# Kernel optimization log

Hardware: AMD Instinct MI355X
Metric: run time of the kernel (lower is better)

Reference implementation:

```python
import jax, jax.numpy as jnp
import numpy as np

N_GENE, N_DRUG = 20000, 3000
D_GENE, D_DRUG = 1024, 512
H = [256, 128]
E_GG, E_DD, E_DT = 600000, 120000, 150000
P_DROP = 0.2


def _dropout(x, key):
    # F.dropout(p=0.2, training=True) with a fixed key for determinism
    keep = jax.random.bernoulli(key, 1.0 - P_DROP, x.shape)
    return jnp.where(keep, x / (1.0 - P_DROP), 0.0).astype(x.dtype)


def _gcn_norm(x, W, b, edge_index, n):
    src, dst = edge_index[0], edge_index[1]
    loops = jnp.arange(n, dtype=src.dtype)
    src = jnp.concatenate([src, loops])
    dst = jnp.concatenate([dst, loops])
    deg = jax.ops.segment_sum(jnp.ones(src.shape, x.dtype), dst, num_segments=n)
    dinv = jax.lax.rsqrt(deg)  # deg >= 1 thanks to self loops
    xw = x @ W  # [n_src, out]
    msg = xw[src] * (dinv[src] * dinv[dst])[:, None]  # [E+n, out]
    return jax.ops.segment_sum(msg, dst, num_segments=n) + b


def _gcn_plain(x, W, b, edge_index, n_dst):
    # PyG GCNConv(add_self_loops=False, normalize=False): A X W + b (bipartite scatter)
    xw = x @ W
    return jax.ops.segment_sum(xw[edge_index[0]], edge_index[1], num_segments=n_dst) + b


def _l2norm(x):
    # F.normalize(dim=1, p=2), eps=1e-12
    n = jnp.linalg.norm(x, axis=1, keepdims=True)
    return x / jnp.maximum(n, 1e-12)


def setup_inputs() -> dict:
    key = jax.random.key(0)
    ks = jax.random.split(key, 32)
    inp = {}
    inp["gene_feat"] = jax.random.normal(ks[0], (N_GENE, D_GENE), jnp.float32)
    inp["drug_feat"] = jax.random.normal(ks[1], (N_DRUG, D_DRUG), jnp.float32)
    inp["ei_gg"] = jax.random.randint(ks[2], (2, E_GG), 0, N_GENE)
    inp["ei_dd"] = jax.random.randint(ks[3], (2, E_DD), 0, N_DRUG)
    # drug_target: messages from drug (src row) to gene (dst row)
    inp["ei_dt"] = jnp.stack([jax.random.randint(ks[4], (E_DT,), 0, N_DRUG),
                               jax.random.randint(ks[5], (E_DT,), 0, N_GENE)])
    # target_drug: messages from gene (src row) to drug (dst row)
    inp["ei_td"] = jnp.stack([jax.random.randint(ks[6], (E_DT,), 0, N_GENE),
                               jax.random.randint(ks[7], (E_DT,), 0, N_DRUG)])
    dims_in = {"gg": D_GENE, "dd": D_DRUG, "dt": D_DRUG, "td": D_GENE}
    i = 8
    for l, h in enumerate(H):
        for et in ["gg", "dd", "dt", "td"]:
            din = dims_in[et] if l == 0 else H[l - 1]
            s = float(1.0 / np.sqrt(din))
            inp[f"W{l}_{et}"] = jax.random.uniform(ks[i], (din, h), jnp.float32, -s, s)
            i += 1
            inp[f"b{l}_{et}"] = jnp.zeros((h,), jnp.float32)
    return inp


def reference(gene_feat, drug_feat, ei_gg, ei_dd, ei_dt, ei_td,
              W0_gg, b0_gg, W0_dd, b0_dd, W0_dt, b0_dt, W0_td, b0_td,
              W1_gg, b1_gg, W1_dd, b1_dd, W1_dt, b1_dt, W1_td, b1_td):
    dk = jax.random.split(jax.random.key(42), 8)
    layers = [
        ((W0_gg, b0_gg), (W0_dd, b0_dd), (W0_dt, b0_dt), (W0_td, b0_td)),
        ((W1_gg, b1_gg), (W1_dd, b1_dd), (W1_dt, b1_dt), (W1_td, b1_td)),
    ]
    xg, xd = gene_feat, drug_feat
    k = 0
    for (Wgg, bgg), (Wdd, bdd), (Wdt, bdt), (Wtd, btd) in layers:
        gg = jax.nn.relu(_gcn_norm(_dropout(xg, dk[k + 0]), Wgg, bgg, ei_gg, N_GENE))
        dd = jax.nn.relu(_gcn_norm(_dropout(xd, dk[k + 1]), Wdd, bdd, ei_dd, N_DRUG))
        dt = jax.nn.relu(_gcn_plain(_dropout(xd, dk[k + 2]), Wdt, bdt, ei_dt, N_GENE))
        td = jax.nn.relu(_gcn_plain(_dropout(xg, dk[k + 3]), Wtd, btd, ei_td, N_DRUG))
        # per-edge-type L2 normalize, then sum contributions per node type
        xg = _l2norm(gg) + _l2norm(dt)
        xd = _l2norm(dd) + _l2norm(td)
        k += 4
    # concat node-type outputs: genes first, drugs second -> [N_GENE+N_DRUG, H[-1]]
    return jnp.concatenate([xg, xd], axis=0)
```

## Files before the change

### kernel.cpp

```cpp
#include <hip/hip_runtime.h>
#include <stdint.h>

#define N_GENE 20000
#define N_DRUG 3000
#define D_GENE 1024
#define D_DRUG 512
#define H0 256
#define H1 128
#define E_GG 600000
#define E_DD 120000
#define E_DT 150000

typedef __attribute__((ext_vector_type(8))) short bf16x8;
typedef __attribute__((ext_vector_type(4))) float f32x4;

__host__ __device__ inline uint32_t rotl32(uint32_t x, int d) {
#ifdef __HIP_DEVICE_COMPILE__
    return __builtin_amdgcn_alignbit(x, x, 32 - d);
#else
    return (x << d) | (x >> (32 - d));
#endif
}

__host__ __device__ inline void tf2x32(uint32_t k0, uint32_t k1, uint32_t x0, uint32_t x1,
                                       uint32_t& o0, uint32_t& o1) {
    uint32_t ks2 = k0 ^ k1 ^ 0x1BD11BDAu;
    x0 += k0; x1 += k1;
#define TFR(r) { x0 += x1; x1 = rotl32(x1, r); x1 ^= x0; }
    TFR(13) TFR(15) TFR(26) TFR(6)
    x0 += k1; x1 += ks2 + 1u;
    TFR(17) TFR(29) TFR(16) TFR(24)
    x0 += ks2; x1 += k0 + 2u;
    TFR(13) TFR(15) TFR(26) TFR(6)
    x0 += k0; x1 += k1 + 3u;
    TFR(17) TFR(29) TFR(16) TFR(24)
    x0 += k1; x1 += ks2 + 4u;
    TFR(13) TFR(15) TFR(26) TFR(6)
    x0 += ks2; x1 += k0 + 5u;
#undef TFR
    o0 = x0; o1 = x1;
}

__device__ inline short f2bf(float f) {
    uint32_t u = __float_as_uint(f);
    uint32_t r = (u + 0x7FFFu + ((u >> 16) & 1u)) >> 16;
    return (short)r;
}
__device__ inline float bf_lo(uint32_t u) { return __uint_as_float(u << 16); }
__device__ inline float bf_hi(uint32_t u) { return __uint_as_float(u & 0xFFFF0000u); }

#define CUM_E0 600000u
#define CUM_E1 720000u
#define CUM_E2 870000u
#define CUM_E3 1020000u

struct Cast4P {
    unsigned c0, c1, c2, c3;
    uint32_t k0a, k1a, k0b, k1b, k0c, k1c, k0d, k1d;
};
__global__ __launch_bounds__(256) void cast4_kernel(
    const float* __restrict__ Xg, const float* __restrict__ Xd,
    short* __restrict__ Am, Cast4P P, int castBlocks,
    const int* __restrict__ gg, const int* __restrict__ dd,
    const int* __restrict__ dt, const int* __restrict__ td, int* __restrict__ cnt) {
    int bx = blockIdx.x;
    if (bx >= castBlocks) {
        unsigned e = (unsigned)(bx - castBlocks) * 256u + threadIdx.x;
        if (e >= CUM_E3) return;
        const int* dsts; unsigned base, noff;
        if (e >= CUM_E2)      { dsts = td + E_DT; base = CUM_E2; noff = 43000; }
        else if (e >= CUM_E1) { dsts = dt + E_DT; base = CUM_E1; noff = 23000; }
        else if (e >= CUM_E0) { dsts = dd + E_DD; base = CUM_E0; noff = 20000; }
        else                  { dsts = gg + E_GG; base = 0;      noff = 0; }
        atomicAdd(&cnt[noff + dsts[e - base]], 1);
        return;
    }
    unsigned j = ((unsigned)bx * 256u + threadIdx.x) * 8u;
    if (j >= P.c3) return;
    unsigned base; uint32_t k0, k1; const float* X;
    if (j >= P.c2)      { base = P.c2; k0 = P.k0d; k1 = P.k1d; X = Xd; }
    else if (j >= P.c1) { base = P.c1; k0 = P.k0c; k1 = P.k1c; X = Xd; }
    else if (j >= P.c0) { base = P.c0; k0 = P.k0b; k1 = P.k1b; X = Xg; }
    else                { base = 0u;   k0 = P.k0a; k1 = P.k1a; X = Xg; }
    unsigned local = j - base;
    float4 xa = *(const float4*)(X + local);
    float4 xb = *(const float4*)(X + local + 4);
    float xv[8] = {xa.x, xa.y, xa.z, xa.w, xb.x, xb.y, xb.z, xb.w};
    union { short s[8]; uint4 u; } st;
#pragma unroll
    for (int i = 0; i < 8; i++) {
        uint32_t a, b;
        tf2x32(k0, k1, 0u, local + (unsigned)i, a, b);
        uint32_t bits = a ^ b;
        st.s[i] = ((bits >> 9) < 6710887u) ? f2bf(xv[i] * 1.25f) : (short)0;
    }
    *(uint4*)(Am + j) = st.u;
}

__global__ __launch_bounds__(1024) void scan_p1(const int* __restrict__ cnt,
                                                int* __restrict__ tmp, int* __restrict__ bsum) {
    __shared__ int buf[1024];
    int tid = threadIdx.x;
    int i = blockIdx.x * 1024 + tid;
    int v = (i < 46000) ? cnt[i] : 0;
    buf[tid] = v;
    __syncthreads();
    for (int off = 1; off < 1024; off <<= 1) {
        int t = (tid >= off) ? buf[tid - off] : 0;
        __syncthreads();
        buf[tid] += t;
        __syncthreads();
    }
    if (i < 46000) tmp[i] = buf[tid];
    if (tid == 1023) bsum[blockIdx.x] = buf[1023];
}

__global__ void scan_p2(int* __restrict__ bsum) {
    int lane = threadIdx.x;
    int v = (lane < 45) ? bsum[lane] : 0;
    int orig = v;
    for (int off = 1; off < 64; off <<= 1) {
        int t = __shfl_up(v, off, 64);
        if (lane >= off) v += t;
    }
    if (lane < 45) bsum[lane] = v - orig;
}

__global__ __launch_bounds__(1024) void scan_p3(const int* __restrict__ cnt,
                                                const int* __restrict__ tmp,
                                                const int* __restrict__ bsum,
                                                int* __restrict__ rpall, int* __restrict__ pos,
                                                float* __restrict__ dinv_g,
                                                float* __restrict__ dinv_d) {
    int i = blockIdx.x * 1024 + threadIdx.x;
    if (i < 46000) {
        int g = tmp[i] - cnt[i] + bsum[blockIdx.x];
        rpall[i] = g;
        pos[i] = g;
        if (i < 20000) dinv_g[i] = 1.0f / sqrtf((float)cnt[i] + 1.0f);
        else if (i < 23000) dinv_d[i - 20000] = 1.0f / sqrtf((float)cnt[i] + 1.0f);
    }
    if (i == 0) rpall[46000] = (int)CUM_E3;
}

struct CastT4P {
    unsigned c0, c1, c2, c3;
    int lgK0, lgK1, lgK2, lgK3;
    int N;
};
__global__ __launch_bounds__(256) void fillcastT_kernel(
    const int* __restrict__ gg, const int* __restrict__ dd,
    const int* __restrict__ dt, const int* __restrict__ td,
    int* __restrict__ pos, int* __restrict__ col,
    const float* __restrict__ W0, const float* __restrict__ W1,
    const float* __restrict__ W2, const float* __restrict__ W3,
    short* __restrict__ Wt, CastT4P P, int fillBlocks) {
    int bx = blockIdx.x;
    if (bx < fillBlocks) {
        unsigned e = (unsigned)bx * 256u + threadIdx.x;
        if (e >= CUM_E3) return;
        const int* ei; unsigned base, noff; int E;
        if (e >= CUM_E2)      { ei = td; base = CUM_E2; noff = 43000; E = E_DT; }
        else if (e >= CUM_E1) { ei = dt; base = CUM_E1; noff = 23000; E = E_DT; }
        else if (e >= CUM_E0) { ei = dd; base = CUM_E0; noff = 20000; E = E_DD; }
        else                  { ei = gg; base = 0;      noff = 0;     E = E_GG; }
        unsigned local = e - base;
        int src = ei[local], dst = ei[E + local];
        int p = atomicAdd(&pos[noff + dst], 1);
        col[p] = src;
        return;
    }
    unsigned idx = (unsigned)(bx - fillBlocks) * 256u + threadIdx.x;
    if (idx >= P.c3) return;
    unsigned base; const float* W; int lgK;
    if (idx >= P.c2)      { base = P.c2; W = W3; lgK = P.lgK3; }
    else if (idx >= P.c1) { base = P.c1; W = W2; lgK = P.lgK2; }
    else if (idx >= P.c0) { base = P.c0; W = W1; lgK = P.lgK1; }
    else                  { base = 0u;   W = W0; lgK = P.lgK0; }
    unsigned local = idx - base;
    unsigned n = local >> lgK, k = local & ((1u << lgK) - 1u);
    Wt[idx] = f2bf(W[(size_t)k * P.N + n]);
}

__global__ __launch_bounds__(256) void castT4_kernel(
    const float* __restrict__ W0, const float* __restrict__ W1,
    const float* __restrict__ W2, const float* __restrict__ W3,
    short* __restrict__ Wt, CastT4P P) {
    unsigned idx = blockIdx.x * 256u + threadIdx.x;
    if (idx >= P.c3) return;
    unsigned base; const float* W; int lgK;
    if (idx >= P.c2)      { base = P.c2; W = W3; lgK = P.lgK3; }
    else if (idx >= P.c1) { base = P.c1; W = W2; lgK = P.lgK2; }
    else if (idx >= P.c0) { base = P.c0; W = W1; lgK = P.lgK1; }
    else                  { base = 0u;   W = W0; lgK = P.lgK0; }
    unsigned local = idx - base;
    unsigned n = local >> lgK, k = local & ((1u << lgK) - 1u);
    Wt[idx] = f2bf(W[(size_t)k * P.N + n]);
}

struct GDesc { unsigned aoff, boff, coff; const float* rs; int M, K, mb0; };
#define LDP 72
__global__ __launch_bounds__(256) void gemm4_kernel(
    const short* __restrict__ Ab, const short* __restrict__ Wb, short* __restrict__ Cb,
    GDesc d0, GDesc d1, GDesc d2, GDesc d3, int N) {
    __shared__ short As[64 * LDP];
    __shared__ short Bs[64 * LDP];
    GDesc d;
    int bx = blockIdx.x;
    if (bx >= d3.mb0) d = d3;
    else if (bx >= d2.mb0) d = d2;
    else if (bx >= d1.mb0) d = d1;
    else d = d0;
    bx -= d.mb0;
    const short* A = Ab + d.aoff;
    const short* Bt = Wb + d.boff;
    short* C = Cb + d.coff;
    const int M = d.M, K = d.K;

    int tid = threadIdx.x;
    int lane = tid & 63;
    int w = tid >> 6;
    int m = lane & 15, kb = lane >> 4;
    int m0w = (w >> 1) * 32, n0w = (w & 1) * 32;
    int gm = bx * 64, gn = blockIdx.y * 64;

    int flat0 = tid, flat1 = tid + 256;
    int ar0 = flat0 >> 3, ac0 = (flat0 & 7) * 8;
    int ar1 = flat1 >> 3, ac1 = (flat1 & 7) * 8;
    int agr0 = min(gm + ar0, M - 1), agr1 = min(gm + ar1, M - 1);
    const short* pa0 = A + (size_t)agr0 * K + ac0;
    const short* pa1 = A + (size_t)agr1 * K + ac1;
    const short* pb0 = Bt + (size_t)(gn + ar0) * K + ac0;
    const short* pb1 = Bt + (size_t)(gn + ar1) * K + ac1;

    f32x4 acc[2][2];
#pragma unroll
    for (int i = 0; i < 2; i++)
#pragma unroll
        for (int j = 0; j < 2; j++) acc[i][j] = (f32x4){0.f, 0.f, 0.f, 0.f};

    uint4 ra0 = *(const uint4*)pa0;
    uint4 ra1 = *(const uint4*)pa1;
    uint4 rb0 = *(const uint4*)pb0;
    uint4 rb1 = *(const uint4*)pb1;

    int nt = K >> 6;
    for (int t = 0; t < nt; ++t) {
        __syncthreads();
        *(uint4*)&As[ar0 * LDP + ac0] = ra0;
        *(uint4*)&As[ar1 * LDP + ac1] = ra1;
        *(uint4*)&Bs[ar0 * LDP + ac0] = rb0;
        *(uint4*)&Bs[ar1 * LDP + ac1] = rb1;
        __syncthreads();
        if (t + 1 < nt) {
            int kt = (t + 1) << 6;
            ra0 = *(const uint4*)(pa0 + kt);
            ra1 = *(const uint4*)(pa1 + kt);
            rb0 = *(const uint4*)(pb0 + kt);
            rb1 = *(const uint4*)(pb1 + kt);
        }
#pragma unroll
        for (int ks = 0; ks < 2; ++ks) {
            bf16x8 a0 = *(const bf16x8*)&As[(m0w + m) * LDP + ks * 32 + kb * 8];
            bf16x8 a1 = *(const bf16x8*)&As[(m0w + 16 + m) * LDP + ks * 32 + kb * 8];
            bf16x8 b0 = *(const bf16x8*)&Bs[(n0w + m) * LDP + ks * 32 + kb * 8];
            bf16x8 b1 = *(const bf16x8*)&Bs[(n0w + 16 + m) * LDP + ks * 32 + kb * 8];
            acc[0][0] = __builtin_amdgcn_mfma_f32_16x16x32_bf16(a0, b0, acc[0][0], 0, 0, 0);
            acc[0][1] = __builtin_amdgcn_mfma_f32_16x16x32_bf16(a0, b1, acc[0][1], 0, 0, 0);
            acc[1][0] = __builtin_amdgcn_mfma_f32_16x16x32_bf16(a1, b0, acc[1][0], 0, 0, 0);
            acc[1][1] = __builtin_amdgcn_mfma_f32_16x16x32_bf16(a1, b1, acc[1][1], 0, 0, 0);
        }
    }
#pragma unroll
    for (int mf = 0; mf < 2; ++mf)
#pragma unroll
        for (int j = 0; j < 4; ++j) {
            int r = gm + m0w + mf * 16 + kb * 4 + j;
            if (r < M) {
                float s = d.rs ? d.rs[r] : 1.0f;
#pragma unroll
                for (int nf = 0; nf < 2; ++nf)
                    C[(size_t)r * N + gn + n0w + nf * 16 + m] = f2bf(acc[mf][nf][j] * s);
            }
        }
}

template <int F>
__global__ __launch_bounds__(256) void agg2_kernel(
    const short* __restrict__ XWa, const int* __restrict__ rpa,
    const float* __restrict__ dinv, const float* __restrict__ ba,
    const short* __restrict__ XWb2, const int* __restrict__ rpb,
    const float* __restrict__ bb, const int* __restrict__ col,
    float* __restrict__ out, int n_dst) {
    const int h = 64 * F;
    int lane = threadIdx.x & 63;
    int row = blockIdx.x * 4 + (threadIdx.x >> 6);
    if (row >= n_dst) return;
    int c0 = lane * F;
    float acc[F], va[F];

#pragma unroll
    for (int i = 0; i < F; i++) acc[i] = 0.f;
    {
        if constexpr (F == 4) {
            uint2 u = *(const uint2*)(XWa + (size_t)row * h + c0);
            acc[0] += bf_lo(u.x); acc[1] += bf_hi(u.x);
            acc[2] += bf_lo(u.y); acc[3] += bf_hi(u.y);
        } else {
            uint32_t u = *(const uint32_t*)(XWa + (size_t)row * h + c0);
            acc[0] += bf_lo(u); acc[1] += bf_hi(u);
        }
        int s0 = rpa[row], s1 = rpa[row + 1];
        int p = s0;
        for (; p + 8 <= s1; p += 8) {
            int c[8];
#pragma unroll
            for (int i = 0; i < 8; i++) c[i] = col[p + i];
            if constexpr (F == 4) {
                uint2 g[8];
#pragma unroll
                for (int i = 0; i < 8; i++) g[i] = *(const uint2*)(XWa + (size_t)c[i] * h + c0);
#pragma unroll
                for (int i = 0; i < 8; i++) {
                    acc[0] += bf_lo(g[i].x); acc[1] += bf_hi(g[i].x);
                    acc[2] += bf_lo(g[i].y); acc[3] += bf_hi(g[i].y);
                }
            } else {
                uint32_t g[8];
#pragma unroll
                for (int i = 0; i < 8; i++) g[i] = *(const uint32_t*)(XWa + (size_t)c[i] * h + c0);
#pragma unroll
                for (int i = 0; i < 8; i++) { acc[0] += bf_lo(g[i]); acc[1] += bf_hi(g[i]); }
            }
        }
        for (; p < s1; p++) {
            int s = col[p];
            if constexpr (F == 4) {
                uint2 u = *(const uint2*)(XWa + (size_t)s * h + c0);
                acc[0] += bf_lo(u.x); acc[1] += bf_hi(u.x);
                acc[2] += bf_lo(u.y); acc[3] += bf_hi(u.y);
            } else {
                uint32_t u = *(const uint32_t*)(XWa + (size_t)s * h + c0);
                acc[0] += bf_lo(u); acc[1] += bf_hi(u);
            }
        }
    }
    float mul = dinv[row];
    float ssa = 0.f;
#pragma unroll
    for (int i = 0; i < F; i++) {
        float v = fmaxf(acc[i] * mul + ba[c0 + i], 0.f);
        va[i] = v;
        ssa += v * v;
    }

#pragma unroll
    for (int i = 0; i < F; i++) acc[i] = 0.f;
    {
        int s0 = rpb[row], s1 = rpb[row + 1];
        int p = s0;
        for (; p + 8 <= s1; p += 8) {
            int c[8];
#pragma unroll
            for (int i = 0; i < 8; i++) c[i] = col[p + i];
            if constexpr (F == 4) {
                uint2 g[8];
#pragma unroll
                for (int i = 0; i < 8; i++) g[i] = *(const uint2*)(XWb2 + (size_t)c[i] * h + c0);
#pragma unroll
                for (int i = 0; i < 8; i++) {
                    acc[0] += bf_lo(g[i].x); acc[1] += bf_hi(g[i].x);
                    acc[2] += bf_lo(g[i].y); acc[3] += bf_hi(g[i].y);
                }
            } else {
                uint32_t g[8];
#pragma unroll
                for (int i = 0; i < 8; i++) g[i] = *(const uint32_t*)(XWb2 + (size_t)c[i] * h + c0);
#pragma unroll
                for (int i = 0; i < 8; i++) { acc[0] += bf_lo(g[i]); acc[1] += bf_hi(g[i]); }
            }
        }
        for (; p < s1; p++) {
            int s = col[p];
            if constexpr (F == 4) {
                uint2 u = *(const uint2*)(XWb2 + (size_t)s * h + c0);
                acc[0] += bf_lo(u.x); acc[1] += bf_hi(u.x);
                acc[2] += bf_lo(u.y); acc[3] += bf_hi(u.y);
            } else {
                uint32_t u = *(const uint32_t*)(XWb2 + (size_t)s * h + c0);
                acc[0] += bf_lo(u); acc[1] += bf_hi(u);
            }
        }
    }
    float ssb = 0.f;
#pragma unroll
    for (int i = 0; i < F; i++) {
        float v = fmaxf(acc[i] + bb[c0 + i], 0.f);
        acc[i] = v;
        ssb += v * v;
    }

#pragma unroll
    for (int off = 32; off >= 1; off >>= 1) {
        ssa += __shfl_xor(ssa, off, 64);
        ssb += __shfl_xor(ssb, off, 64);
    }
    float sa = 1.0f / fmaxf(sqrtf(ssa), 1e-12f);
    float sb = 1.0f / fmaxf(sqrtf(ssb), 1e-12f);
    float* orow = out + (size_t)row * h + c0;
    if constexpr (F == 4) {
        *(float4*)orow = make_float4(va[0] * sa + acc[0] * sb, va[1] * sa + acc[1] * sb,
                                     va[2] * sa + acc[2] * sb, va[3] * sa + acc[3] * sb);
    } else {
        *(float2*)orow = make_float2(va[0] * sa + acc[0] * sb, va[1] * sa + acc[1] * sb);
    }
}

extern "C" void kernel_launch(void* const* d_in, const int* in_sizes, int n_in,
                              void* d_out, int out_size, void* d_ws, size_t ws_size,
                              hipStream_t stream) {
    const float* gene = (const float*)d_in[0];
    const float* drug = (const float*)d_in[1];
    const int* ei_gg = (const int*)d_in[2];
    const int* ei_dd = (const int*)d_in[3];
    const int* ei_dt = (const int*)d_in[4];
    const int* ei_td = (const int*)d_in[5];
    const float* W0gg = (const float*)d_in[6];  const float* b0gg = (const float*)d_in[7];
    const float* W0dd = (const float*)d_in[8];  const float* b0dd = (const float*)d_in[9];
    const float* W0dt = (const float*)d_in[10]; const float* b0dt = (const float*)d_in[11];
    const float* W0td = (const float*)d_in[12]; const float* b0td = (const float*)d_in[13];
    const float* W1gg = (const float*)d_in[14]; const float* b1gg = (const float*)d_in[15];
    const float* W1dd = (const float*)d_in[16]; const float* b1dd = (const float*)d_in[17];
    const float* W1dt = (const float*)d_in[18]; const float* b1dt = (const float*)d_in[19];
    const float* W1td = (const float*)d_in[20]; const float* b1td = (const float*)d_in[21];

    uint32_t dk[8][2];
    for (uint32_t i = 0; i < 8; i++) tf2x32(0u, 42u, 0u, i, dk[i][0], dk[i][1]);

    char* p = (char*)d_ws;
    auto take = [&](size_t bytes) -> void* {
        void* r = (void*)p;
        p += (bytes + 255) & ~(size_t)255;
        return r;
    };
    short* Am   = (short*)take(sizeof(short) * 44032000ULL);
    short* XW   = (short*)take(sizeof(short) * 11776000ULL);
    short* Wt   = (short*)take(sizeof(short) * 786432ULL);
    float* xg1  = (float*)take(sizeof(float) * (size_t)N_GENE * H0);
    float* xd1  = (float*)take(sizeof(float) * (size_t)N_DRUG * H0);
    float* dinv_g = (float*)take(sizeof(float) * N_GENE);
    float* dinv_d = (float*)take(sizeof(float) * N_DRUG);
    int* cnt   = (int*)take(4 * 46000);
    int* tmp   = (int*)take(4 * 46000);
    int* bsum  = (int*)take(4 * 64);
    int* pos   = (int*)take(4 * 46000);
    int* rpall = (int*)take(4 * 46001);
    int* col   = (int*)take(4 * 1020000);

    const int* rp_gg = rpall;
    const int* rp_dd = rpall + 20000;
    const int* rp_dt = rpall + 23000;
    const int* rp_td = rpall + 43000;

    hipMemsetAsync(cnt, 0, 4 * 46000, stream);

    {
        Cast4P cp = {20480000u, 40960000u, 42496000u, 44032000u,
                     dk[0][0], dk[0][1], dk[3][0], dk[3][1],
                     dk[1][0], dk[1][1], dk[2][0], dk[2][1]};
        int castBlocks = 44032000 / 8 / 256;
        int countBlocks = (1020000 + 255) / 256;
        cast4_kernel<<<castBlocks + countBlocks, 256, 0, stream>>>(
            gene, drug, Am, cp, castBlocks, ei_gg, ei_dd, ei_dt, ei_td, cnt);
        scan_p1<<<45, 1024, 0, stream>>>(cnt, tmp, bsum);
        scan_p2<<<1, 64, 0, stream>>>(bsum);
        scan_p3<<<45, 1024, 0, stream>>>(cnt, tmp, bsum, rpall, pos, dinv_g, dinv_d);
        CastT4P tp = {262144u, 524288u, 655360u, 786432u, 10, 10, 9, 9, H0};
        int fillBlocks = (1020000 + 255) / 256;
        fillcastT_kernel<<<fillBlocks + (786432 + 255) / 256, 256, 0, stream>>>(
            ei_gg, ei_dd, ei_dt, ei_td, pos, col,
            W0gg, W0td, W0dd, W0dt, Wt, tp, fillBlocks);
        GDesc g0 = {0u,        0u,      0u,        dinv_g,  N_GENE, 1024, 0};
        GDesc g1 = {20480000u, 262144u, 5120000u,  nullptr, N_GENE, 1024, 313};
        GDesc g2 = {40960000u, 524288u, 10240000u, dinv_d,  N_DRUG, 512,  626};
        GDesc g3 = {42496000u, 655360u, 11008000u, nullptr, N_DRUG, 512,  673};
        gemm4_kernel<<<dim3(720, H0 / 64), 256, 0, stream>>>(Am, Wt, XW, g0, g1, g2, g3, H0);
        agg2_kernel<4><<<(N_GENE + 3) / 4, 256, 0, stream>>>(
            XW, rp_gg, dinv_g, b0gg, XW + 11008000, rp_dt, b0dt, col, xg1, N_GENE);
        agg2_kernel<4><<<(N_DRUG + 3) / 4, 256, 0, stream>>>(
            XW + 10240000, rp_dd, dinv_d, b0dd, XW + 5120000, rp_td, b0td, col, xd1, N_DRUG);
    }

    {
        Cast4P cp = {5120000u, 10240000u, 11008000u, 11776000u,
                     dk[4][0], dk[4][1], dk[7][0], dk[7][1],
                     dk[5][0], dk[5][1], dk[6][0], dk[6][1]};
        int castBlocks = 11776000 / 8 / 256;
        cast4_kernel<<<castBlocks, 256, 0, stream>>>(
            xg1, xd1, Am, cp, castBlocks, nullptr, nullptr, nullptr, nullptr, nullptr);
        CastT4P tp = {32768u, 65536u, 98304u, 131072u, 8, 8, 8, 8, H1};
        castT4_kernel<<<(131072 + 255) / 256, 256, 0, stream>>>(W1gg, W1td, W1dd, W1dt, Wt, tp);
        GDesc g0 = {0u,        0u,     0u,        dinv_g,  N_GENE, 256, 0};
        GDesc g1 = {5120000u,  32768u, 5120000u,  nullptr, N_GENE, 256, 313};
        GDesc g2 = {10240000u, 65536u, 10240000u, dinv_d,  N_DRUG, 256, 626};
        GDesc g3 = {11008000u, 98304u, 11008000u, nullptr, N_DRUG, 256, 673};
        gemm4_kernel<<<dim3(720, H1 / 64), 256, 0, stream>>>(Am, Wt, XW, g0, g1, g2, g3, H1);
        float* og = (float*)d_out;
        float* od = og + (size_t)N_GENE * H1;
        agg2_kernel<2><<<(N_GENE + 3) / 4, 256, 0, stream>>>(
            XW, rp_gg, dinv_g, b1gg, XW + 11008000, rp_dt, b1dt, col, og, N_GENE);
        agg2_kernel<2><<<(N_DRUG + 3) / 4, 256, 0, stream>>>(
            XW + 10240000, rp_dd, dinv_d, b1dd, XW + 5120000, rp_td, b1td, col, od, N_DRUG);
    }
}
```

Baseline: 421.3 us.

## Fuse dropout mask and bf16 cast into GEMM A-tile loads with full-N tiles

Removes the separate cast kernel that wrote a large dropout-masked bf16 copy of the activations. The GEMM now reads the fp32 features directly and computes the Threefry dropout mask inside the A-tile load. Each block covers the full output width (256 or 128) with 512 threads, so every A row is loaded once instead of once per 64-column tile. The cost is that the Threefry hashing now sits inside the GEMM's load path, fp32 A loads are twice as wide, and register use per thread goes up.

```diff
diff --git a/kernel.cpp b/kernel.cpp
--- a/kernel.cpp
+++ b/kernel.cpp
@@ -49,42 +49,7 @@
 __device__ inline float bf_lo(uint32_t u) { return __uint_as_float(u << 16); }
 __device__ inline float bf_hi(uint32_t u) { return __uint_as_float(u & 0xFFFF0000u); }
 
-#define CUM_E0 600000u
-#define CUM_E1 720000u
-#define CUM_E2 870000u
-#define CUM_E3 1020000u
-
-struct Cast4P {
-    unsigned c0, c1, c2, c3;
-    uint32_t k0a, k1a, k0b, k1b, k0c, k1c, k0d, k1d;
-};
-__global__ __launch_bounds__(256) void cast4_kernel(
-    const float* __restrict__ Xg, const float* __restrict__ Xd,
-    short* __restrict__ Am, Cast4P P, int castBlocks,
-    const int* __restrict__ gg, const int* __restrict__ dd,
-    const int* __restrict__ dt, const int* __restrict__ td, int* __restrict__ cnt) {
-    int bx = blockIdx.x;
-    if (bx >= castBlocks) {
-        unsigned e = (unsigned)(bx - castBlocks) * 256u + threadIdx.x;
-        if (e >= CUM_E3) return;
-        const int* dsts; unsigned base, noff;
-        if (e >= CUM_E2)      { dsts = td + E_DT; base = CUM_E2; noff = 43000; }
-        else if (e >= CUM_E1) { dsts = dt + E_DT; base = CUM_E1; noff = 23000; }
-        else if (e >= CUM_E0) { dsts = dd + E_DD; base = CUM_E0; noff = 20000; }
-        else                  { dsts = gg + E_GG; base = 0;      noff = 0; }
-        atomicAdd(&cnt[noff + dsts[e - base]], 1);
-        return;
-    }
-    unsigned j = ((unsigned)bx * 256u + threadIdx.x) * 8u;
-    if (j >= P.c3) return;
-    unsigned base; uint32_t k0, k1; const float* X;
-    if (j >= P.c2)      { base = P.c2; k0 = P.k0d; k1 = P.k1d; X = Xd; }
-    else if (j >= P.c1) { base = P.c1; k0 = P.k0c; k1 = P.k1c; X = Xd; }
-    else if (j >= P.c0) { base = P.c0; k0 = P.k0b; k1 = P.k1b; X = Xg; }
-    else                { base = 0u;   k0 = P.k0a; k1 = P.k1a; X = Xg; }
-    unsigned local = j - base;
-    float4 xa = *(const float4*)(X + local);
-    float4 xb = *(const float4*)(X + local + 4);
+__device__ inline uint4 maskpack8(float4 xa, float4 xb, unsigned local, uint32_t k0, uint32_t k1) {
     float xv[8] = {xa.x, xa.y, xa.z, xa.w, xb.x, xb.y, xb.z, xb.w};
     union { short s[8]; uint4 u; } st;
 #pragma unroll
@@ -94,7 +59,25 @@
         uint32_t bits = a ^ b;
         st.s[i] = ((bits >> 9) < 6710887u) ? f2bf(xv[i] * 1.25f) : (short)0;
     }
-    *(uint4*)(Am + j) = st.u;
+    return st.u;
+}
+
+#define CUM_E0 600000u
+#define CUM_E1 720000u
+#define CUM_E2 870000u
+#define CUM_E3 1020000u
+
+__global__ void count4_kernel(const int* __restrict__ gg, const int* __restrict__ dd,
+                              const int* __restrict__ dt, const int* __restrict__ td,
+                              int* __restrict__ cnt) {
+    unsigned e = blockIdx.x * 256u + threadIdx.x;
+    if (e >= CUM_E3) return;
+    const int* dsts; unsigned base, noff;
+    if (e >= CUM_E2)      { dsts = td + E_DT; base = CUM_E2; noff = 43000; }
+    else if (e >= CUM_E1) { dsts = dt + E_DT; base = CUM_E1; noff = 23000; }
+    else if (e >= CUM_E0) { dsts = dd + E_DD; base = CUM_E0; noff = 20000; }
+    else                  { dsts = gg + E_GG; base = 0;      noff = 0; }
+    atomicAdd(&cnt[noff + dsts[e - base]], 1);
 }
 
 __global__ __launch_bounds__(1024) void scan_p1(const int* __restrict__ cnt,
@@ -198,77 +181,86 @@
     Wt[idx] = f2bf(W[(size_t)k * P.N + n]);
 }
 
-struct GDesc { unsigned aoff, boff, coff; const float* rs; int M, K, mb0; };
+struct GDescF { const float* X; unsigned boff, coff; const float* rs; int M, K, mb0; uint32_t k0, k1; };
 #define LDP 72
-__global__ __launch_bounds__(256) void gemm4_kernel(
-    const short* __restrict__ Ab, const short* __restrict__ Wb, short* __restrict__ Cb,
-    GDesc d0, GDesc d1, GDesc d2, GDesc d3, int N) {
+template <int BN>
+__global__ __launch_bounds__(512) void gemm4f_kernel(
+    const short* __restrict__ Wb, short* __restrict__ Cb,
+    GDescF d0, GDescF d1, GDescF d2, GDescF d3) {
+    constexpr int WN = BN / 4;
+    constexpr int NF = WN / 16;
+    constexpr int SB = BN / 64;
     __shared__ short As[64 * LDP];
-    __shared__ short Bs[64 * LDP];
-    GDesc d;
+    __shared__ short Bs[BN * LDP];
+    GDescF d;
     int bx = blockIdx.x;
     if (bx >= d3.mb0) d = d3;
     else if (bx >= d2.mb0) d = d2;
     else if (bx >= d1.mb0) d = d1;
     else d = d0;
     bx -= d.mb0;
-    const short* A = Ab + d.aoff;
+    const int M = d.M, K = d.K;
     const short* Bt = Wb + d.boff;
     short* C = Cb + d.coff;
-    const int M = d.M, K = d.K;
 
     int tid = threadIdx.x;
-    int lane = tid & 63;
-    int w = tid >> 6;
+    int lane = tid & 63, w = tid >> 6;
     int m = lane & 15, kb = lane >> 4;
-    int m0w = (w >> 1) * 32, n0w = (w & 1) * 32;
-    int gm = bx * 64, gn = blockIdx.y * 64;
-
-    int flat0 = tid, flat1 = tid + 256;
-    int ar0 = flat0 >> 3, ac0 = (flat0 & 7) * 8;
-    int ar1 = flat1 >> 3, ac1 = (flat1 & 7) * 8;
-    int agr0 = min(gm + ar0, M - 1), agr1 = min(gm + ar1, M - 1);
-    const short* pa0 = A + (size_t)agr0 * K + ac0;
-    const short* pa1 = A + (size_t)agr1 * K + ac1;
-    const short* pb0 = Bt + (size_t)(gn + ar0) * K + ac0;
-    const short* pb1 = Bt + (size_t)(gn + ar1) * K + ac1;
-
-    f32x4 acc[2][2];
+    int m0w = (w >> 2) * 32, n0w = (w & 3) * WN;
+    int gm = bx * 64;
+
+    int ar = tid >> 3, ac = (tid & 7) * 8;
+    int agr = min(gm + ar, M - 1);
+    const float* pax = d.X + (size_t)agr * K + ac;
+    unsigned alocal = (unsigned)agr * (unsigned)K + (unsigned)ac;
+
+    int brr[SB], bcc[SB];
+    const short* pb[SB];
+#pragma unroll
+    for (int i = 0; i < SB; i++) {
+        int flat = tid + 512 * i;
+        brr[i] = flat >> 3; bcc[i] = (flat & 7) * 8;
+        pb[i] = Bt + (size_t)brr[i] * K + bcc[i];
+    }
+
+    f32x4 acc[2][NF];
 #pragma unroll
     for (int i = 0; i < 2; i++)
 #pragma unroll
-        for (int j = 0; j < 2; j++) acc[i][j] = (f32x4){0.f, 0.f, 0.f, 0.f};
-
-    uint4 ra0 = *(const uint4*)pa0;
-    uint4 ra1 = *(const uint4*)pa1;
-    uint4 rb0 = *(const uint4*)pb0;
-    uint4 rb1 = *(const uint4*)pb1;
+        for (int j = 0; j < NF; j++) acc[i][j] = (f32x4){0.f, 0.f, 0.f, 0.f};
+
+    float4 xa = *(const float4*)pax;
+    float4 xb = *(const float4*)(pax + 4);
+    uint4 rb[SB];
+#pragma unroll
+    for (int i = 0; i < SB; i++) rb[i] = *(const uint4*)pb[i];
+    uint4 a8 = maskpack8(xa, xb, alocal, d.k0, d.k1);
 
     int nt = K >> 6;
     for (int t = 0; t < nt; ++t) {
         __syncthreads();
-        *(uint4*)&As[ar0 * LDP + ac0] = ra0;
-        *(uint4*)&As[ar1 * LDP + ac1] = ra1;
-        *(uint4*)&Bs[ar0 * LDP + ac0] = rb0;
-        *(uint4*)&Bs[ar1 * LDP + ac1] = rb1;
+        *(uint4*)&As[ar * LDP + ac] = a8;
+#pragma unroll
+        for (int i = 0; i < SB; i++) *(uint4*)&Bs[brr[i] * LDP + bcc[i]] = rb[i];
         __syncthreads();
         if (t + 1 < nt) {
             int kt = (t + 1) << 6;
-            ra0 = *(const uint4*)(pa0 + kt);
-            ra1 = *(const uint4*)(pa1 + kt);
-            rb0 = *(const uint4*)(pb0 + kt);
-            rb1 = *(const uint4*)(pb1 + kt);
+            xa = *(const float4*)(pax + kt);
+            xb = *(const float4*)(pax + kt + 4);
+#pragma unroll
+            for (int i = 0; i < SB; i++) rb[i] = *(const uint4*)(pb[i] + kt);
+            a8 = maskpack8(xa, xb, alocal + (unsigned)kt, d.k0, d.k1);
         }
 #pragma unroll
         for (int ks = 0; ks < 2; ++ks) {
             bf16x8 a0 = *(const bf16x8*)&As[(m0w + m) * LDP + ks * 32 + kb * 8];
             bf16x8 a1 = *(const bf16x8*)&As[(m0w + 16 + m) * LDP + ks * 32 + kb * 8];
-            bf16x8 b0 = *(const bf16x8*)&Bs[(n0w + m) * LDP + ks * 32 + kb * 8];
-            bf16x8 b1 = *(const bf16x8*)&Bs[(n0w + 16 + m) * LDP + ks * 32 + kb * 8];
-            acc[0][0] = __builtin_amdgcn_mfma_f32_16x16x32_bf16(a0, b0, acc[0][0], 0, 0, 0);
-            acc[0][1] = __builtin_amdgcn_mfma_f32_16x16x32_bf16(a0, b1, acc[0][1], 0, 0, 0);
-            acc[1][0] = __builtin_amdgcn_mfma_f32_16x16x32_bf16(a1, b0, acc[1][0], 0, 0, 0);
-            acc[1][1] = __builtin_amdgcn_mfma_f32_16x16x32_bf16(a1, b1, acc[1][1], 0, 0, 0);
+#pragma unroll
+            for (int nf = 0; nf < NF; nf++) {
+                bf16x8 bf = *(const bf16x8*)&Bs[(n0w + nf * 16 + m) * LDP + ks * 32 + kb * 8];
+                acc[0][nf] = __builtin_amdgcn_mfma_f32_16x16x32_bf16(a0, bf, acc[0][nf], 0, 0, 0);
+                acc[1][nf] = __builtin_amdgcn_mfma_f32_16x16x32_bf16(a1, bf, acc[1][nf], 0, 0, 0);
+            }
         }
     }
 #pragma unroll
@@ -279,8 +271,8 @@
             if (r < M) {
                 float s = d.rs ? d.rs[r] : 1.0f;
 #pragma unroll
-                for (int nf = 0; nf < 2; ++nf)
-                    C[(size_t)r * N + gn + n0w + nf * 16 + m] = f2bf(acc[mf][nf][j] * s);
+                for (int nf = 0; nf < NF; ++nf)
+                    C[(size_t)r * BN + n0w + nf * 16 + m] = f2bf(acc[mf][nf][j] * s);
             }
         }
 }
@@ -443,7 +435,6 @@
         p += (bytes + 255) & ~(size_t)255;
         return r;
     };
-    short* Am   = (short*)take(sizeof(short) * 44032000ULL);
     short* XW   = (short*)take(sizeof(short) * 11776000ULL);
     short* Wt   = (short*)take(sizeof(short) * 786432ULL);
     float* xg1  = (float*)take(sizeof(float) * (size_t)N_GENE * H0);
@@ -463,28 +454,22 @@
     const int* rp_td = rpall + 43000;
 
     hipMemsetAsync(cnt, 0, 4 * 46000, stream);
+    count4_kernel<<<(1020000 + 255) / 256, 256, 0, stream>>>(ei_gg, ei_dd, ei_dt, ei_td, cnt);
+    scan_p1<<<45, 1024, 0, stream>>>(cnt, tmp, bsum);
+    scan_p2<<<1, 64, 0, stream>>>(bsum);
+    scan_p3<<<45, 1024, 0, stream>>>(cnt, tmp, bsum, rpall, pos, dinv_g, dinv_d);
+    CastT4P tp0 = {262144u, 524288u, 655360u, 786432u, 10, 10, 9, 9, H0};
+    int fillBlocks = (1020000 + 255) / 256;
+    fillcastT_kernel<<<fillBlocks + (786432 + 255) / 256, 256, 0, stream>>>(
+        ei_gg, ei_dd, ei_dt, ei_td, pos, col,
+        W0gg, W0td, W0dd, W0dt, Wt, tp0, fillBlocks);
 
     {
-        Cast4P cp = {20480000u, 40960000u, 42496000u, 44032000u,
-                     dk[0][0], dk[0][1], dk[3][0], dk[3][1],
-                     dk[1][0], dk[1][1], dk[2][0], dk[2][1]};
-        int castBlocks = 44032000 / 8 / 256;
-        int countBlocks = (1020000 + 255) / 256;
-        cast4_kernel<<<castBlocks + countBlocks, 256, 0, stream>>>(
-            gene, drug, Am, cp, castBlocks, ei_gg, ei_dd, ei_dt, ei_td, cnt);
-        scan_p1<<<45, 1024, 0, stream>>>(cnt, tmp, bsum);
-        scan_p2<<<1, 64, 0, stream>>>(bsum);
-        scan_p3<<<45, 1024, 0, stream>>>(cnt, tmp, bsum, rpall, pos, dinv_g, dinv_d);
-        CastT4P tp = {262144u, 524288u, 655360u, 786432u, 10, 10, 9, 9, H0};
-        int fillBlocks = (1020000 + 255) / 256;
-        fillcastT_kernel<<<fillBlocks + (786432 + 255) / 256, 256, 0, stream>>>(
-            ei_gg, ei_dd, ei_dt, ei_td, pos, col,
-            W0gg, W0td, W0dd, W0dt, Wt, tp, fillBlocks);
-        GDesc g0 = {0u,        0u,      0u,        dinv_g,  N_GENE, 1024, 0};
-        GDesc g1 = {20480000u, 262144u, 5120000u,  nullptr, N_GENE, 1024, 313};
-        GDesc g2 = {40960000u, 524288u, 10240000u, dinv_d,  N_DRUG, 512,  626};
-        GDesc g3 = {42496000u, 655360u, 11008000u, nullptr, N_DRUG, 512,  673};
-        gemm4_kernel<<<dim3(720, H0 / 64), 256, 0, stream>>>(Am, Wt, XW, g0, g1, g2, g3, H0);
+        GDescF g0 = {gene, 0u,      0u,        dinv_g,  N_GENE, 1024, 0,   dk[0][0], dk[0][1]};
+        GDescF g1 = {gene, 262144u, 5120000u,  nullptr, N_GENE, 1024, 313, dk[3][0], dk[3][1]};
+        GDescF g2 = {drug, 524288u, 10240000u, dinv_d,  N_DRUG, 512,  626, dk[1][0], dk[1][1]};
+        GDescF g3 = {drug, 655360u, 11008000u, nullptr, N_DRUG, 512,  673, dk[2][0], dk[2][1]};
+        gemm4f_kernel<256><<<720, 512, 0, stream>>>(Wt, XW, g0, g1, g2, g3);
         agg2_kernel<4><<<(N_GENE + 3) / 4, 256, 0, stream>>>(
             XW, rp_gg, dinv_g, b0gg, XW + 11008000, rp_dt, b0dt, col, xg1, N_GENE);
         agg2_kernel<4><<<(N_DRUG + 3) / 4, 256, 0, stream>>>(
@@ -492,19 +477,13 @@
     }
 
     {
-        Cast4P cp = {5120000u, 10240000u, 11008000u, 11776000u,
-                     dk[4][0], dk[4][1], dk[7][0], dk[7][1],
-                     dk[5][0], dk[5][1], dk[6][0], dk[6][1]};
-        int castBlocks = 11776000 / 8 / 256;
-        cast4_kernel<<<castBlocks, 256, 0, stream>>>(
-            xg1, xd1, Am, cp, castBlocks, nullptr, nullptr, nullptr, nullptr, nullptr);
-        CastT4P tp = {32768u, 65536u, 98304u, 131072u, 8, 8, 8, 8, H1};
-        castT4_kernel<<<(131072 + 255) / 256, 256, 0, stream>>>(W1gg, W1td, W1dd, W1dt, Wt, tp);
-        GDesc g0 = {0u,        0u,     0u,        dinv_g,  N_GENE, 256, 0};
-        GDesc g1 = {5120000u,  32768u, 5120000u,  nullptr, N_GENE, 256, 313};
-        GDesc g2 = {10240000u, 65536u, 10240000u, dinv_d,  N_DRUG, 256, 626};
-        GDesc g3 = {11008000u, 98304u, 11008000u, nullptr, N_DRUG, 256, 673};
-        gemm4_kernel<<<dim3(720, H1 / 64), 256, 0, stream>>>(Am, Wt, XW, g0, g1, g2, g3, H1);
+        CastT4P tp1 = {32768u, 65536u, 98304u, 131072u, 8, 8, 8, 8, H1};
+        castT4_kernel<<<(131072 + 255) / 256, 256, 0, stream>>>(W1gg, W1td, W1dd, W1dt, Wt, tp1);
+        GDescF g0 = {xg1, 0u,     0u,        dinv_g,  N_GENE, 256, 0,   dk[4][0], dk[4][1]};
+        GDescF g1 = {xg1, 32768u, 5120000u,  nullptr, N_GENE, 256, 313, dk[7][0], dk[7][1]};
+        GDescF g2 = {xd1, 65536u, 10240000u, dinv_d,  N_DRUG, 256, 626, dk[5][0], dk[5][1]};
+        GDescF g3 = {xd1, 98304u, 11008000u, nullptr, N_DRUG, 256, 673, dk[6][0], dk[6][1]};
+        gemm4f_kernel<128><<<720, 512, 0, stream>>>(Wt, XW, g0, g1, g2, g3);
         float* og = (float*)d_out;
         float* od = og + (size_t)N_GENE * H1;
         agg2_kernel<2><<<(N_GENE + 3) / 4, 256, 0, stream>>>(
```

Result: slower. 477.7 us (+13.4%).

## Merge gene/drug aggregation launches, fold layer-1 weight cast in, move dropout scale to GEMM

Applied to the files above, without the earlier changes.

The two per-node-type aggregation kernels are merged into one launch per layer, and the layer-1 weight transpose-cast is appended as extra blocks of the layer-0 aggregation launch, using a separate Wt1 buffer. The dropout 1/(1-p) factor moves out of the elementwise cast and into the GEMM epilogue scale, and the cast packs bf16 pairs directly. This removes several kernel launches and per-element multiplies. The cost is a heavier combined kernel and slightly different rounding, since bf16 rounding now happens before the 1.25 scale.

```diff
diff --git a/kernel.cpp b/kernel.cpp
--- a/kernel.cpp
+++ b/kernel.cpp
@@ -41,13 +41,23 @@
     o0 = x0; o1 = x1;
 }
 
+__device__ inline float bf_lo(uint32_t u) { return __uint_as_float(u << 16); }
+__device__ inline float bf_hi(uint32_t u) { return __uint_as_float(u & 0xFFFF0000u); }
+
+__device__ inline uint32_t drnd(float x, unsigned idx, uint32_t k0, uint32_t k1) {
+    uint32_t a, b;
+    tf2x32(k0, k1, 0u, idx, a, b);
+    uint32_t bits = a ^ b;
+    uint32_t u = __float_as_uint(x);
+    uint32_t r = ((u + 0x7FFFu + ((u >> 16) & 1u)) >> 16) & 0xFFFFu;
+    return ((bits >> 9) < 6710887u) ? r : 0u;
+}
+
 __device__ inline short f2bf(float f) {
     uint32_t u = __float_as_uint(f);
     uint32_t r = (u + 0x7FFFu + ((u >> 16) & 1u)) >> 16;
     return (short)r;
 }
-__device__ inline float bf_lo(uint32_t u) { return __uint_as_float(u << 16); }
-__device__ inline float bf_hi(uint32_t u) { return __uint_as_float(u & 0xFFFF0000u); }
 
 #define CUM_E0 600000u
 #define CUM_E1 720000u
@@ -85,16 +95,11 @@
     unsigned local = j - base;
     float4 xa = *(const float4*)(X + local);
     float4 xb = *(const float4*)(X + local + 4);
-    float xv[8] = {xa.x, xa.y, xa.z, xa.w, xb.x, xb.y, xb.z, xb.w};
-    union { short s[8]; uint4 u; } st;
-#pragma unroll
-    for (int i = 0; i < 8; i++) {
-        uint32_t a, b;
-        tf2x32(k0, k1, 0u, local + (unsigned)i, a, b);
-        uint32_t bits = a ^ b;
-        st.s[i] = ((bits >> 9) < 6710887u) ? f2bf(xv[i] * 1.25f) : (short)0;
-    }
-    *(uint4*)(Am + j) = st.u;
+    uint32_t w0 = drnd(xa.x, local + 0u, k0, k1) | (drnd(xa.y, local + 1u, k0, k1) << 16);
+    uint32_t w1 = drnd(xa.z, local + 2u, k0, k1) | (drnd(xa.w, local + 3u, k0, k1) << 16);
+    uint32_t w2 = drnd(xb.x, local + 4u, k0, k1) | (drnd(xb.y, local + 5u, k0, k1) << 16);
+    uint32_t w3 = drnd(xb.z, local + 6u, k0, k1) | (drnd(xb.w, local + 7u, k0, k1) << 16);
+    *(uint4*)(Am + j) = make_uint4(w0, w1, w2, w3);
 }
 
 __global__ __launch_bounds__(1024) void scan_p1(const int* __restrict__ cnt,
@@ -148,6 +153,20 @@
     int lgK0, lgK1, lgK2, lgK3;
     int N;
 };
+__device__ inline void castT_body(unsigned idx, const float* W0, const float* W1,
+                                  const float* W2, const float* W3,
+                                  short* __restrict__ Wt, const CastT4P& P) {
+    if (idx >= P.c3) return;
+    unsigned base; const float* W; int lgK;
+    if (idx >= P.c2)      { base = P.c2; W = W3; lgK = P.lgK3; }
+    else if (idx >= P.c1) { base = P.c1; W = W2; lgK = P.lgK2; }
+    else if (idx >= P.c0) { base = P.c0; W = W1; lgK = P.lgK1; }
+    else                  { base = 0u;   W = W0; lgK = P.lgK0; }
+    unsigned local = idx - base;
+    unsigned n = local >> lgK, k = local & ((1u << lgK) - 1u);
+    Wt[idx] = f2bf(W[(size_t)k * P.N + n]);
+}
+
 __global__ __launch_bounds__(256) void fillcastT_kernel(
     const int* __restrict__ gg, const int* __restrict__ dd,
     const int* __restrict__ dt, const int* __restrict__ td,
@@ -170,32 +189,7 @@
         col[p] = src;
         return;
     }
-    unsigned idx = (unsigned)(bx - fillBlocks) * 256u + threadIdx.x;
-    if (idx >= P.c3) return;
-    unsigned base; const float* W; int lgK;
-    if (idx >= P.c2)      { base = P.c2; W = W3; lgK = P.lgK3; }
-    else if (idx >= P.c1) { base = P.c1; W = W2; lgK = P.lgK2; }
-    else if (idx >= P.c0) { base = P.c0; W = W1; lgK = P.lgK1; }
-    else                  { base = 0u;   W = W0; lgK = P.lgK0; }
-    unsigned local = idx - base;
-    unsigned n = local >> lgK, k = local & ((1u << lgK) - 1u);
-    Wt[idx] = f2bf(W[(size_t)k * P.N + n]);
-}
-
-__global__ __launch_bounds__(256) void castT4_kernel(
-    const float* __restrict__ W0, const float* __restrict__ W1,
-    const float* __restrict__ W2, const float* __restrict__ W3,
-    short* __restrict__ Wt, CastT4P P) {
-    unsigned idx = blockIdx.x * 256u + threadIdx.x;
-    if (idx >= P.c3) return;
-    unsigned base; const float* W; int lgK;
-    if (idx >= P.c2)      { base = P.c2; W = W3; lgK = P.lgK3; }
-    else if (idx >= P.c1) { base = P.c1; W = W2; lgK = P.lgK2; }
-    else if (idx >= P.c0) { base = P.c0; W = W1; lgK = P.lgK1; }
-    else                  { base = 0u;   W = W0; lgK = P.lgK0; }
-    unsigned local = idx - base;
-    unsigned n = local >> lgK, k = local & ((1u << lgK) - 1u);
-    Wt[idx] = f2bf(W[(size_t)k * P.N + n]);
+    castT_body((unsigned)(bx - fillBlocks) * 256u + threadIdx.x, W0, W1, W2, W3, Wt, P);
 }
 
 struct GDesc { unsigned aoff, boff, coff; const float* rs; int M, K, mb0; };
@@ -277,7 +271,7 @@
         for (int j = 0; j < 4; ++j) {
             int r = gm + m0w + mf * 16 + kb * 4 + j;
             if (r < M) {
-                float s = d.rs ? d.rs[r] : 1.0f;
+                float s = (d.rs ? d.rs[r] : 1.0f) * 1.25f;
 #pragma unroll
                 for (int nf = 0; nf < 2; ++nf)
                     C[(size_t)r * N + gn + n0w + nf * 16 + m] = f2bf(acc[mf][nf][j] * s);
@@ -285,17 +279,15 @@
         }
 }
 
+struct AggP {
+    const short* XWa; const int* rpa; const float* dinv; const float* ba;
+    const short* XWb; const int* rpb; const float* bb;
+    float* out; int n_dst;
+};
+
 template <int F>
-__global__ __launch_bounds__(256) void agg2_kernel(
-    const short* __restrict__ XWa, const int* __restrict__ rpa,
-    const float* __restrict__ dinv, const float* __restrict__ ba,
-    const short* __restrict__ XWb2, const int* __restrict__ rpb,
-    const float* __restrict__ bb, const int* __restrict__ col,
-    float* __restrict__ out, int n_dst) {
+__device__ inline void agg_body(const AggP& P, const int* __restrict__ col, int row, int lane) {
     const int h = 64 * F;
-    int lane = threadIdx.x & 63;
-    int row = blockIdx.x * 4 + (threadIdx.x >> 6);
-    if (row >= n_dst) return;
     int c0 = lane * F;
     float acc[F], va[F];
 
@@ -303,14 +295,14 @@
     for (int i = 0; i < F; i++) acc[i] = 0.f;
     {
         if constexpr (F == 4) {
-            uint2 u = *(const uint2*)(XWa + (size_t)row * h + c0);
+            uint2 u = *(const uint2*)(P.XWa + (size_t)row * h + c0);
             acc[0] += bf_lo(u.x); acc[1] += bf_hi(u.x);
             acc[2] += bf_lo(u.y); acc[3] += bf_hi(u.y);
         } else {
-            uint32_t u = *(const uint32_t*)(XWa + (size_t)row * h + c0);
+            uint32_t u = *(const uint32_t*)(P.XWa + (size_t)row * h + c0);
             acc[0] += bf_lo(u); acc[1] += bf_hi(u);
         }
-        int s0 = rpa[row], s1 = rpa[row + 1];
+        int s0 = P.rpa[row], s1 = P.rpa[row + 1];
         int p = s0;
         for (; p + 8 <= s1; p += 8) {
             int c[8];
@@ -319,7 +311,7 @@
             if constexpr (F == 4) {
                 uint2 g[8];
 #pragma unroll
-                for (int i = 0; i < 8; i++) g[i] = *(const uint2*)(XWa + (size_t)c[i] * h + c0);
+                for (int i = 0; i < 8; i++) g[i] = *(const uint2*)(P.XWa + (size_t)c[i] * h + c0);
 #pragma unroll
                 for (int i = 0; i < 8; i++) {
                     acc[0] += bf_lo(g[i].x); acc[1] += bf_hi(g[i].x);
@@ -328,7 +320,7 @@
             } else {
                 uint32_t g[8];
 #pragma unroll
-                for (int i = 0; i < 8; i++) g[i] = *(const uint32_t*)(XWa + (size_t)c[i] * h + c0);
+                for (int i = 0; i < 8; i++) g[i] = *(const uint32_t*)(P.XWa + (size_t)c[i] * h + c0);
 #pragma unroll
                 for (int i = 0; i < 8; i++) { acc[0] += bf_lo(g[i]); acc[1] += bf_hi(g[i]); }
             }
@@ -336,20 +328,20 @@
         for (; p < s1; p++) {
             int s = col[p];
             if constexpr (F == 4) {
-                uint2 u = *(const uint2*)(XWa + (size_t)s * h + c0);
+                uint2 u = *(const uint2*)(P.XWa + (size_t)s * h + c0);
                 acc[0] += bf_lo(u.x); acc[1] += bf_hi(u.x);
                 acc[2] += bf_lo(u.y); acc[3] += bf_hi(u.y);
             } else {
-                uint32_t u = *(const uint32_t*)(XWa + (size_t)s * h + c0);
+                uint32_t u = *(const uint32_t*)(P.XWa + (size_t)s * h + c0);
                 acc[0] += bf_lo(u); acc[1] += bf_hi(u);
             }
         }
     }
-    float mul = dinv[row];
+    float mul = P.dinv[row];
     float ssa = 0.f;
 #pragma unroll
     for (int i = 0; i < F; i++) {
-        float v = fmaxf(acc[i] * mul + ba[c0 + i], 0.f);
+        float v = fmaxf(acc[i] * mul + P.ba[c0 + i], 0.f);
         va[i] = v;
         ssa += v * v;
     }
@@ -357,7 +349,7 @@
 #pragma unroll
     for (int i = 0; i < F; i++) acc[i] = 0.f;
     {
-        int s0 = rpb[row], s1 = rpb[row + 1];
+        int s0 = P.rpb[row], s1 = P.rpb[row + 1];
         int p = s0;
         for (; p + 8 <= s1; p += 8) {
             int c[8];
@@ -366,7 +358,7 @@
             if constexpr (F == 4) {
                 uint2 g[8];
 #pragma unroll
-                for (int i = 0; i < 8; i++) g[i] = *(const uint2*)(XWb2 + (size_t)c[i] * h + c0);
+                for (int i = 0; i < 8; i++) g[i] = *(const uint2*)(P.XWb + (size_t)c[i] * h + c0);
 #pragma unroll
                 for (int i = 0; i < 8; i++) {
                     acc[0] += bf_lo(g[i].x); acc[1] += bf_hi(g[i].x);
@@ -375,7 +367,7 @@
             } else {
                 uint32_t g[8];
 #pragma unroll
-                for (int i = 0; i < 8; i++) g[i] = *(const uint32_t*)(XWb2 + (size_t)c[i] * h + c0);
+                for (int i = 0; i < 8; i++) g[i] = *(const uint32_t*)(P.XWb + (size_t)c[i] * h + c0);
 #pragma unroll
                 for (int i = 0; i < 8; i++) { acc[0] += bf_lo(g[i]); acc[1] += bf_hi(g[i]); }
             }
@@ -383,11 +375,11 @@
         for (; p < s1; p++) {
             int s = col[p];
             if constexpr (F == 4) {
-                uint2 u = *(const uint2*)(XWb2 + (size_t)s * h + c0);
+                uint2 u = *(const uint2*)(P.XWb + (size_t)s * h + c0);
                 acc[0] += bf_lo(u.x); acc[1] += bf_hi(u.x);
                 acc[2] += bf_lo(u.y); acc[3] += bf_hi(u.y);
             } else {
-                uint32_t u = *(const uint32_t*)(XWb2 + (size_t)s * h + c0);
+                uint32_t u = *(const uint32_t*)(P.XWb + (size_t)s * h + c0);
                 acc[0] += bf_lo(u); acc[1] += bf_hi(u);
             }
         }
@@ -395,7 +387,7 @@
     float ssb = 0.f;
 #pragma unroll
     for (int i = 0; i < F; i++) {
-        float v = fmaxf(acc[i] + bb[c0 + i], 0.f);
+        float v = fmaxf(acc[i] + P.bb[c0 + i], 0.f);
         acc[i] = v;
         ssb += v * v;
     }
@@ -407,12 +399,32 @@
     }
     float sa = 1.0f / fmaxf(sqrtf(ssa), 1e-12f);
     float sb = 1.0f / fmaxf(sqrtf(ssb), 1e-12f);
-    float* orow = out + (size_t)row * h + c0;
+    float* orow = P.out + (size_t)row * h + c0;
     if constexpr (F == 4) {
         *(float4*)orow = make_float4(va[0] * sa + acc[0] * sb, va[1] * sa + acc[1] * sb,
                                      va[2] * sa + acc[2] * sb, va[3] * sa + acc[3] * sb);
     } else {
         *(float2*)orow = make_float2(va[0] * sa + acc[0] * sb, va[1] * sa + acc[1] * sb);
+    }
+}
+
+template <int F, bool TAIL>
+__global__ __launch_bounds__(256) void agg2x_kernel(
+    AggP pg, AggP pd, const int* __restrict__ col, int geneBlocks, int aggBlocks,
+    const float* W0, const float* W1, const float* W2, const float* W3,
+    short* Wt, CastT4P tp) {
+    int bx = blockIdx.x;
+    if (TAIL && bx >= aggBlocks) {
+        castT_body((unsigned)(bx - aggBlocks) * 256u + threadIdx.x, W0, W1, W2, W3, Wt, tp);
+        return;
+    }
+    int lane = threadIdx.x & 63;
+    if (bx < geneBlocks) {
+        int row = bx * 4 + (threadIdx.x >> 6);
+        if (row < pg.n_dst) agg_body<F>(pg, col, row, lane);
+    } else {
+        int row = (bx - geneBlocks) * 4 + (threadIdx.x >> 6);
+        if (row < pd.n_dst) agg_body<F>(pd, col, row, lane);
     }
 }
 
@@ -445,7 +457,8 @@
     };
     short* Am   = (short*)take(sizeof(short) * 44032000ULL);
     short* XW   = (short*)take(sizeof(short) * 11776000ULL);
-    short* Wt   = (short*)take(sizeof(short) * 786432ULL);
+    short* Wt0  = (short*)take(sizeof(short) * 786432ULL);
+    short* Wt1  = (short*)take(sizeof(short) * 131072ULL);
     float* xg1  = (float*)take(sizeof(float) * (size_t)N_GENE * H0);
     float* xd1  = (float*)take(sizeof(float) * (size_t)N_DRUG * H0);
     float* dinv_g = (float*)take(sizeof(float) * N_GENE);
@@ -475,20 +488,24 @@
         scan_p1<<<45, 1024, 0, stream>>>(cnt, tmp, bsum);
         scan_p2<<<1, 64, 0, stream>>>(bsum);
         scan_p3<<<45, 1024, 0, stream>>>(cnt, tmp, bsum, rpall, pos, dinv_g, dinv_d);
-        CastT4P tp = {262144u, 524288u, 655360u, 786432u, 10, 10, 9, 9, H0};
+        CastT4P tp0 = {262144u, 524288u, 655360u, 786432u, 10, 10, 9, 9, H0};
         int fillBlocks = (1020000 + 255) / 256;
         fillcastT_kernel<<<fillBlocks + (786432 + 255) / 256, 256, 0, stream>>>(
             ei_gg, ei_dd, ei_dt, ei_td, pos, col,
-            W0gg, W0td, W0dd, W0dt, Wt, tp, fillBlocks);
+            W0gg, W0td, W0dd, W0dt, Wt0, tp0, fillBlocks);
+
         GDesc g0 = {0u,        0u,      0u,        dinv_g,  N_GENE, 1024, 0};
         GDesc g1 = {20480000u, 262144u, 5120000u,  nullptr, N_GENE, 1024, 313};
         GDesc g2 = {40960000u, 524288u, 10240000u, dinv_d,  N_DRUG, 512,  626};
         GDesc g3 = {42496000u, 655360u, 11008000u, nullptr, N_DRUG, 512,  673};
-        gemm4_kernel<<<dim3(720, H0 / 64), 256, 0, stream>>>(Am, Wt, XW, g0, g1, g2, g3, H0);
-        agg2_kernel<4><<<(N_GENE + 3) / 4, 256, 0, stream>>>(
-            XW, rp_gg, dinv_g, b0gg, XW + 11008000, rp_dt, b0dt, col, xg1, N_GENE);
-        agg2_kernel<4><<<(N_DRUG + 3) / 4, 256, 0, stream>>>(
-            XW + 10240000, rp_dd, dinv_d, b0dd, XW + 5120000, rp_td, b0td, col, xd1, N_DRUG);
+        gemm4_kernel<<<dim3(720, H0 / 64), 256, 0, stream>>>(Am, Wt0, XW, g0, g1, g2, g3, H0);
+
+        AggP pg = {XW, rp_gg, dinv_g, b0gg, XW + 11008000, rp_dt, b0dt, xg1, N_GENE};
+        AggP pd = {XW + 10240000, rp_dd, dinv_d, b0dd, XW + 5120000, rp_td, b0td, xd1, N_DRUG};
+        CastT4P tp1 = {32768u, 65536u, 98304u, 131072u, 8, 8, 8, 8, H1};
+        int geneBlocks = (N_GENE + 3) / 4, aggBlocks = geneBlocks + (N_DRUG + 3) / 4;
+        agg2x_kernel<4, true><<<aggBlocks + (131072 + 255) / 256, 256, 0, stream>>>(
+            pg, pd, col, geneBlocks, aggBlocks, W1gg, W1td, W1dd, W1dt, Wt1, tp1);
     }
 
     {
@@ -498,18 +515,20 @@
         int castBlocks = 11776000 / 8 / 256;
         cast4_kernel<<<castBlocks, 256, 0, stream>>>(
             xg1, xd1, Am, cp, castBlocks, nullptr, nullptr, nullptr, nullptr, nullptr);
-        CastT4P tp = {32768u, 65536u, 98304u, 131072u, 8, 8, 8, 8, H1};
-        castT4_kernel<<<(131072 + 255) / 256, 256, 0, stream>>>(W1gg, W1td, W1dd, W1dt, Wt, tp);
         GDesc g0 = {0u,        0u,     0u,        dinv_g,  N_GENE, 256, 0};
         GDesc g1 = {5120000u,  32768u, 5120000u,  nullptr, N_GENE, 256, 313};
         GDesc g2 = {10240000u, 65536u, 10240000u, dinv_d,  N_DRUG, 256, 626};
         GDesc g3 = {11008000u, 98304u, 11008000u, nullptr, N_DRUG, 256, 673};
-        gemm4_kernel<<<dim3(720, H1 / 64), 256, 0, stream>>>(Am, Wt, XW, g0, g1, g2, g3, H1);
+        gemm4_kernel<<<dim3(720, H1 / 64), 256, 0, stream>>>(Am, Wt1, XW, g0, g1, g2, g3, H1);
+
         float* og = (float*)d_out;
         float* od = og + (size_t)N_GENE * H1;
-        agg2_kernel<2><<<(N_GENE + 3) / 4, 256, 0, stream>>>(
-            XW, rp_gg, dinv_g, b1gg, XW + 11008000, rp_dt, b1dt, col, og, N_GENE);
-        agg2_kernel<2><<<(N_DRUG + 3) / 4, 256, 0, stream>>>(
-            XW + 10240000, rp_dd, dinv_d, b1dd, XW + 5120000, rp_td, b1td, col, od, N_DRUG);
-    }
-}
+        AggP pg = {XW, rp_gg, dinv_g, b1gg, XW + 11008000, rp_dt, b1dt, og, N_GENE};
+        AggP pd = {XW + 10240000, rp_dd, dinv_d, b1dd, XW + 5120000, rp_td, b1td, od, N_DRUG};
+        CastT4P tpDummy = {0u, 0u, 0u, 0u, 0, 0, 0, 0, 0};
+        int geneBlocks = (N_GENE + 3) / 4, aggBlocks = geneBlocks + (N_DRUG + 3) / 4;
+        agg2x_kernel<2, false><<<aggBlocks, 256, 0, stream>>>(
+            pg, pd, col, geneBlocks, aggBlocks,
+            nullptr, nullptr, nullptr, nullptr, nullptr, tpDummy);
+    }
+}
```

New measurement: 405.2 us. 1.04x faster.
